# Kernel tuning notes

Measured on AMD Instinct MI355X. Metric: run time of the kernel, lower is better.

## Reference

```python
import jax, jax.numpy as jnp
import numpy as np

N_HEADS = 16
ROPE_BASE = 10000.0


def _rope_tables(T, head_dim, dtype):
    d2 = head_dim // 2
    inv_freq = 1.0 / (ROPE_BASE ** (jnp.arange(0, head_dim, 2, dtype=jnp.float32) / head_dim))
    t = jnp.arange(T, dtype=jnp.float32)
    freqs = jnp.outer(t, inv_freq)  # [T, d2]
    cos = jnp.cos(freqs)[None, :, None, :].astype(dtype)  # [1,T,1,d2]
    sin = jnp.sin(freqs)[None, :, None, :].astype(dtype)
    return cos, sin


def _apply_rotary(x, cos, sin):
    # x: [B,T,H,D]; rotate halves
    d = x.shape[-1] // 2
    x1, x2 = x[..., :d], x[..., d:]
    return jnp.concatenate([x1 * cos + x2 * sin, -x1 * sin + x2 * cos], axis=-1)


def setup_inputs() -> dict:
    key = jax.random.key(0)
    k1, k2, k3 = jax.random.split(key, 3)
    B, T, C = 2, 2048, 1024
    x = jax.random.normal(k1, (B, T, C), dtype=jnp.float32)
    w_attn = jax.random.normal(k2, (3 * C, C), dtype=jnp.float32) * (1.0 / np.sqrt(C))
    w_proj = jax.random.normal(k3, (C, C), dtype=jnp.float32) * (1.0 / np.sqrt(C))
    return {"x": x, "w_attn": w_attn, "w_proj": w_proj}


def reference(x, w_attn, w_proj):
    B, T, C = x.shape
    H = N_HEADS
    D = C // H
    qkv = jnp.einsum('btc,fc->btf', x, w_attn)  # [B,T,3C]
    q, k, v = jnp.split(qkv, 3, axis=2)
    q = q.reshape(B, T, H, D)
    k = k.reshape(B, T, H, D)
    v = v.reshape(B, T, H, D)
    cos, sin = _rope_tables(T, D, x.dtype)
    q = _apply_rotary(q, cos, sin)
    k = _apply_rotary(k, cos, sin)
    # causal SDPA, scale 1/sqrt(D)
    scale = 1.0 / np.sqrt(D)
    scores = jnp.einsum('bqhd,bkhd->bhqk', q, k) * scale
    causal = jnp.tril(jnp.ones((T, T), dtype=bool))
    scores = jnp.where(causal[None, None], scores, jnp.finfo(scores.dtype).min)
    attn = jax.nn.softmax(scores, axis=-1)
    y = jnp.einsum('bhqk,bkhd->bqhd', attn, v).reshape(B, T, C)
    return jnp.einsum('btc,oc->bto', y, w_proj)
```

## Files before the change

kernel.cpp:

```cpp
#include <hip/hip_runtime.h>
#include <math.h>

typedef __bf16 bf16x8 __attribute__((ext_vector_type(8)));
typedef float f32x4 __attribute__((ext_vector_type(4)));

__device__ __forceinline__ unsigned f2bf(float f) {
    union { float f; unsigned u; } v; v.f = f;
    return (v.u + 0x7FFFu + ((v.u >> 16) & 1u)) >> 16;
}

__device__ __forceinline__ unsigned cvtpk(float a, float b) {
    unsigned r;
    __asm__("v_cvt_pk_bf16_f32 %0, %1, %2" : "=v"(r) : "v"(a), "v"(b));
    return r;
}

__device__ __forceinline__ void gload16(const ushort* g, ushort* l) {
    __builtin_amdgcn_global_load_lds(
        (const __attribute__((address_space(1))) void*)g,
        (__attribute__((address_space(3))) void*)l, 16, 0, 0);
}

__device__ __forceinline__ bool src_is_fp32(const unsigned* s) {
    int sane = 0;
#pragma unroll
    for (int i = 0; i < 64; ++i) {
        unsigned lo = s[i] & 0xFFFFu;
        unsigned e = (lo >> 7) & 0xFF;
        if (lo == 0u || (e >= 100u && e <= 140u)) sane++;
    }
    return sane < 48;
}

__global__ __launch_bounds__(256) void tobf16_all_kernel(
    const unsigned* __restrict__ s0, const unsigned* __restrict__ s1,
    const unsigned* __restrict__ s2,
    ushort* __restrict__ d0, ushort* __restrict__ d1, ushort* __restrict__ d2) {
    const int bx = blockIdx.x;
    const unsigned* src;
    ushort* dst;
    int lb;
    if (bx < 2048)      { src = s0; dst = d0; lb = bx; }
    else if (bx < 3584) { src = s1; dst = d1; lb = bx - 2048; }
    else                { src = s2; dst = d2; lb = bx - 3584; }
    const int i = lb * 2048 + threadIdx.x * 8;
    if (src_is_fp32(src)) {
        const float* fs = (const float*)src;
        float4 f0 = *(const float4*)(fs + i);
        float4 f1 = *(const float4*)(fs + i + 4);
        uint4 o;
        o.x = f2bf(f0.x) | (f2bf(f0.y) << 16);
        o.y = f2bf(f0.z) | (f2bf(f0.w) << 16);
        o.z = f2bf(f1.x) | (f2bf(f1.y) << 16);
        o.w = f2bf(f1.z) | (f2bf(f1.w) << 16);
        *(uint4*)(dst + i) = o;
    } else {
        *(uint4*)(dst + i) = *(const uint4*)((const ushort*)src + i);
    }
}

constexpr int GBM = 128, GBN = 128, GBK = 32;

__global__ __launch_bounds__(256) void gemm_qkv_rope_kernel(
    const ushort* __restrict__ A, const ushort* __restrict__ Bmat,
    ushort* __restrict__ qkvh, int K) {
    __shared__ ushort As[2][GBM * GBK];
    __shared__ ushort Bs[2][GBN * GBK];

    const int tid  = threadIdx.x;
    const int lane = tid & 63;
    const int wv   = tid >> 6;
    const int wm   = (wv >> 1) * 64;
    const int wn   = (wv & 1) * 64;

    const ushort* Ab = A + (size_t)blockIdx.x * GBM * K;
    const ushort* Bb = Bmat + (size_t)blockIdx.y * GBN * K;

    f32x4 acc[4][4];
#pragma unroll
    for (int i = 0; i < 4; i++)
#pragma unroll
        for (int j = 0; j < 4; j++) acc[i][j] = (f32x4){0.f, 0.f, 0.f, 0.f};

    const int srow = tid >> 2;
    const int scol = (tid & 3) * 8;
    const int fr = lane & 15;
    const int fk = (lane >> 4) * 8;
    const int nK = K >> 5;

    gload16(Ab + (size_t)srow * K + scol,        As[0] + wv * 512);
    gload16(Ab + (size_t)(srow + 64) * K + scol, As[0] + wv * 512 + 2048);
    gload16(Bb + (size_t)srow * K + scol,        Bs[0] + wv * 512);
    gload16(Bb + (size_t)(srow + 64) * K + scol, Bs[0] + wv * 512 + 2048);

#pragma unroll 1
    for (int it = 0; it < nK; ++it) {
        const int cur = it & 1;
        __syncthreads();
        if (it + 1 < nK) {
            const int k0 = (it + 1) << 5, nxt = cur ^ 1;
            gload16(Ab + (size_t)srow * K + k0 + scol,        As[nxt] + wv * 512);
            gload16(Ab + (size_t)(srow + 64) * K + k0 + scol, As[nxt] + wv * 512 + 2048);
            gload16(Bb + (size_t)srow * K + k0 + scol,        Bs[nxt] + wv * 512);
            gload16(Bb + (size_t)(srow + 64) * K + k0 + scol, Bs[nxt] + wv * 512 + 2048);
        }
        bf16x8 af[4], bfr[4];
#pragma unroll
        for (int i = 0; i < 4; i++)
            af[i] = *(const bf16x8*)(As[cur] + (wm + i * 16 + fr) * GBK + fk);
#pragma unroll
        for (int j = 0; j < 4; j++)
            bfr[j] = *(const bf16x8*)(Bs[cur] + (wn + j * 16 + fr) * GBK + fk);
#pragma unroll
        for (int i = 0; i < 4; i++)
#pragma unroll
            for (int j = 0; j < 4; j++)
                acc[i][j] = __builtin_amdgcn_mfma_f32_16x16x32_bf16(af[i], bfr[j], acc[i][j], 0, 0, 0);
    }

    const int crow0 = (lane >> 4) * 4;
    const int col0  = blockIdx.y * GBN + wn;
    const int which = col0 >> 10;
    const int hh    = (col0 >> 6) & 15;
    ushort* outp = qkvh + (size_t)which * 4194304 + (size_t)hh * 131072;

    if (which < 2) {
        const float inva = exp2f((float)fr * -0.41524101186f);
        const float invb = exp2f((float)(fr + 16) * -0.41524101186f);
        const float qs = (which == 0) ? 0.125f : 1.0f;
#pragma unroll
        for (int i = 0; i < 4; i++)
#pragma unroll
            for (int r = 0; r < 4; r++) {
                int row = blockIdx.x * GBM + wm + i * 16 + crow0 + r;
                int t = row & 2047;
                size_t ob = ((size_t)(row >> 11)) * 2097152 + (size_t)t * 64;
                float sa, ca, sb, cb;
                __sincosf((float)t * inva, &sa, &ca);
                __sincosf((float)t * invb, &sb, &cb);
                float q0 = acc[i][0][r], q1 = acc[i][1][r];
                float q2 = acc[i][2][r], q3 = acc[i][3][r];
                float n0 = (q0 * ca + q2 * sa) * qs;
                float n1 = (q1 * cb + q3 * sb) * qs;
                float n2 = (q2 * ca - q0 * sa) * qs;
                float n3 = (q3 * cb - q1 * sb) * qs;
                unsigned u01 = cvtpk(n0, n1);
                unsigned u23 = cvtpk(n2, n3);
                outp[ob + fr]      = (ushort)(u01 & 0xFFFFu);
                outp[ob + 16 + fr] = (ushort)(u01 >> 16);
                outp[ob + 32 + fr] = (ushort)(u23 & 0xFFFFu);
                outp[ob + 48 + fr] = (ushort)(u23 >> 16);
            }
    } else {
#pragma unroll
        for (int i = 0; i < 4; i++)
#pragma unroll
            for (int r = 0; r < 4; r++) {
                int row = blockIdx.x * GBM + wm + i * 16 + crow0 + r;
                int t = row & 2047;
                size_t ob = ((size_t)(row >> 11)) * 2097152 + (size_t)t * 64;
                unsigned u01 = cvtpk(acc[i][0][r], acc[i][1][r]);
                unsigned u23 = cvtpk(acc[i][2][r], acc[i][3][r]);
                outp[ob + fr]      = (ushort)(u01 & 0xFFFFu);
                outp[ob + 16 + fr] = (ushort)(u01 >> 16);
                outp[ob + 32 + fr] = (ushort)(u23 & 0xFFFFu);
                outp[ob + 48 + fr] = (ushort)(u23 >> 16);
            }
    }
}

__global__ __launch_bounds__(256) void gemm_bt_kernel(
    const ushort* __restrict__ A, const ushort* __restrict__ Bmat,
    float* __restrict__ C, int M, int N, int K) {
    __shared__ ushort As[2][GBM * GBK];
    __shared__ ushort Bs[2][GBN * GBK];

    const int tid  = threadIdx.x;
    const int lane = tid & 63;
    const int wv   = tid >> 6;
    const int wm   = (wv >> 1) * 64;
    const int wn   = (wv & 1) * 64;

    const ushort* Ab = A + (size_t)blockIdx.x * GBM * K;
    const ushort* Bb = Bmat + (size_t)blockIdx.y * GBN * K;

    f32x4 acc[4][4];
#pragma unroll
    for (int i = 0; i < 4; i++)
#pragma unroll
        for (int j = 0; j < 4; j++) acc[i][j] = (f32x4){0.f, 0.f, 0.f, 0.f};

    const int srow = tid >> 2;
    const int scol = (tid & 3) * 8;
    const int fr = lane & 15;
    const int fk = (lane >> 4) * 8;
    const int nK = K >> 5;

    gload16(Ab + (size_t)srow * K + scol,        As[0] + wv * 512);
    gload16(Ab + (size_t)(srow + 64) * K + scol, As[0] + wv * 512 + 2048);
    gload16(Bb + (size_t)srow * K + scol,        Bs[0] + wv * 512);
    gload16(Bb + (size_t)(srow + 64) * K + scol, Bs[0] + wv * 512 + 2048);

#pragma unroll 1
    for (int it = 0; it < nK; ++it) {
        const int cur = it & 1;
        __syncthreads();
        if (it + 1 < nK) {
            const int k0 = (it + 1) << 5, nxt = cur ^ 1;
            gload16(Ab + (size_t)srow * K + k0 + scol,        As[nxt] + wv * 512);
            gload16(Ab + (size_t)(srow + 64) * K + k0 + scol, As[nxt] + wv * 512 + 2048);
            gload16(Bb + (size_t)srow * K + k0 + scol,        Bs[nxt] + wv * 512);
            gload16(Bb + (size_t)(srow + 64) * K + k0 + scol, Bs[nxt] + wv * 512 + 2048);
        }
        bf16x8 af[4], bfr[4];
#pragma unroll
        for (int i = 0; i < 4; i++)
            af[i] = *(const bf16x8*)(As[cur] + (wm + i * 16 + fr) * GBK + fk);
#pragma unroll
        for (int j = 0; j < 4; j++)
            bfr[j] = *(const bf16x8*)(Bs[cur] + (wn + j * 16 + fr) * GBK + fk);
#pragma unroll
        for (int i = 0; i < 4; i++)
#pragma unroll
            for (int j = 0; j < 4; j++)
                acc[i][j] = __builtin_amdgcn_mfma_f32_16x16x32_bf16(af[i], bfr[j], acc[i][j], 0, 0, 0);
    }

    const int crow0 = (lane >> 4) * 4;
#pragma unroll
    for (int i = 0; i < 4; i++)
#pragma unroll
        for (int j = 0; j < 4; j++)
#pragma unroll
            for (int r = 0; r < 4; r++) {
                int row = blockIdx.x * GBM + wm + i * 16 + crow0 + r;
                int col = blockIdx.y * GBN + wn + j * 16 + fr;
                C[(size_t)row * N + col] = acc[i][j][r];
            }
}

#define NEG_BIG (-1e30f)
constexpr int VT_OFF = 16384;
constexpr int LPV    = 136;
constexpr int PS_OFF = VT_OFF + 2 * 64 * LPV;
constexpr int LPP    = 72;

__global__ __launch_bounds__(1024) void attn_kernel(const ushort* __restrict__ qkvh,
                                                    ushort* __restrict__ y) {
    __shared__ ushort SM[PS_OFF + 16 * 16 * LPP];

    const int tid  = threadIdx.x;
    const int lane = tid & 63;
    const int wv   = tid >> 6;
    const int half = wv >> 3;
    const int wq   = wv & 7;
    const int jb   = half * 4;
    const int pid  = blockIdx.x;
    const int bh   = blockIdx.y;
    const int b    = bh >> 4, h = bh & 15;

    const ushort* qp = qkvh + (size_t)b * 2097152 + (size_t)h * 131072;
    const ushort* kp = qp + 4194304;
    const ushort* vp = qp + 8388608;

    const int fr = lane & 15;
    const int fq = lane >> 4;
    const int fk = fq * 8;

    const int krow = tid >> 3;
    const int kblk = tid & 7;
    const int ksrc = krow * 64 + ((kblk ^ (krow & 7)) << 3);
    const int koff0 = (fq ^ (fr & 7)) << 3;
    const int koff1 = koff0 ^ 32;
    const int vkey = tid & 127;
    const int vd0  = (tid >> 7) * 8;

    ushort* pw = SM + PS_OFF + wv * (16 * LPP);

#pragma unroll 1
    for (int seg = 0; seg < 2; ++seg) {
        const int qb = seg ? (15 - pid) : pid;
        const int nIt = qb + 1;

        __syncthreads();

        gload16(kp + ksrc, SM + wv * 512);
        uint4 vr = *(const uint4*)(vp + (size_t)vkey * 64 + vd0);
        {
            unsigned w[4] = {vr.x, vr.y, vr.z, vr.w};
            ushort* vt0 = SM + VT_OFF;
#pragma unroll
            for (int t = 0; t < 4; ++t) {
                vt0[(vd0 + 2 * t)     * LPV + vkey] = (ushort)(w[t] & 0xFFFFu);
                vt0[(vd0 + 2 * t + 1) * LPV + vkey] = (ushort)(w[t] >> 16);
            }
        }
        if (1 < nIt)
            vr = *(const uint4*)(vp + (size_t)(128 + vkey) * 64 + vd0);

        const int qrow = qb * 128 + wq * 16 + fr;
        bf16x8 qf0 = *(const bf16x8*)(qp + (size_t)qrow * 64 + fk);
        bf16x8 qf1 = *(const bf16x8*)(qp + (size_t)qrow * 64 + 32 + fk);

        f32x4 o[4];
        o[0] = o[1] = o[2] = o[3] = (f32x4){0.f, 0.f, 0.f, 0.f};
        float lsum = 0.f;

#pragma unroll 1
        for (int it = 0; it < nIt; ++it) {
            const int cur = it & 1;
            const int k0 = it * 128;
            const ushort* Ksc = SM + cur * 8192;
            const ushort* Vtc = SM + VT_OFF + cur * (64 * LPV);
            __syncthreads();
            if (it + 1 < nIt) {
                const int nxt = cur ^ 1;
                gload16(kp + (it + 1) * 8192 + ksrc, SM + nxt * 8192 + wv * 512);
                ushort* vtn = SM + VT_OFF + nxt * (64 * LPV);
                unsigned w[4] = {vr.x, vr.y, vr.z, vr.w};
#pragma unroll
                for (int t = 0; t < 4; ++t) {
                    vtn[(vd0 + 2 * t)     * LPV + vkey] = (ushort)(w[t] & 0xFFFFu);
                    vtn[(vd0 + 2 * t + 1) * LPV + vkey] = (ushort)(w[t] >> 16);
                }
                if (it + 2 < nIt)
                    vr = *(const uint4*)(vp + (size_t)(k0 + 256 + vkey) * 64 + vd0);
            }

            f32x4 s[4];
#pragma unroll
            for (int jl = 0; jl < 4; ++jl) {
                const int row = ((jb + jl) * 16 + fr) * 64;
                bf16x8 kf0 = *(const bf16x8*)(Ksc + row + koff0);
                bf16x8 kf1 = *(const bf16x8*)(Ksc + row + koff1);
                f32x4 z = (f32x4){0.f, 0.f, 0.f, 0.f};
                z = __builtin_amdgcn_mfma_f32_16x16x32_bf16(kf0, qf0, z, 0, 0, 0);
                z = __builtin_amdgcn_mfma_f32_16x16x32_bf16(kf1, qf1, z, 0, 0, 0);
                s[jl] = z;
            }
            if (it + 1 < nIt) {
#pragma unroll
                for (int jl = 0; jl < 4; ++jl)
#pragma unroll
                    for (int r = 0; r < 4; ++r) {
                        float p = __expf(s[jl][r]);
                        s[jl][r] = p;
                        lsum += p;
                    }
            } else {
#pragma unroll
                for (int jl = 0; jl < 4; ++jl)
#pragma unroll
                    for (int r = 0; r < 4; ++r) {
                        float v = s[jl][r];
                        if ((k0 + (jb + jl) * 16 + fq * 4 + r) > qrow) v = NEG_BIG;
                        float p = __expf(v);
                        s[jl][r] = p;
                        lsum += p;
                    }
            }

#pragma unroll
            for (int jl = 0; jl < 4; ++jl) {
                uint2 u;
                u.x = cvtpk(s[jl][0], s[jl][1]);
                u.y = cvtpk(s[jl][2], s[jl][3]);
                *(uint2*)(pw + fr * LPP + jl * 16 + fq * 4) = u;
            }
            __asm__ volatile("" ::: "memory");

#pragma unroll
            for (int kl = 0; kl < 2; ++kl) {
                bf16x8 pf = *(const bf16x8*)(pw + fr * LPP + kl * 32 + fk);
                const int vcol = half * 64 + kl * 32 + fk;
#pragma unroll
                for (int j4 = 0; j4 < 4; ++j4) {
                    bf16x8 vf = *(const bf16x8*)(Vtc + (j4 * 16 + fr) * LPV + vcol);
                    o[j4] = __builtin_amdgcn_mfma_f32_16x16x32_bf16(pf, vf, o[j4], 0, 0, 0);
                }
            }
        }

        lsum += __shfl_xor(lsum, 16, 64);
        lsum += __shfl_xor(lsum, 32, 64);

        __syncthreads();
        float* ex = (float*)(SM + PS_OFF) + wq * 1104;
        if (half) {
#pragma unroll
            for (int j4 = 0; j4 < 4; ++j4)
#pragma unroll
                for (int r = 0; r < 4; ++r)
                    ex[lane * 17 + j4 * 4 + r] = o[j4][r];
            if (fq == 0) ex[1088 + fr] = lsum;
        }
        __syncthreads();
        if (!half) {
            float linv[4];
#pragma unroll
            for (int r = 0; r < 4; ++r) {
                float own = __shfl(lsum, fq * 4 + r, 64);
                linv[r] = 1.0f / (own + ex[1088 + fq * 4 + r]);
            }
#pragma unroll
            for (int j4 = 0; j4 < 4; j4 += 2)
#pragma unroll
                for (int r = 0; r < 4; ++r) {
                    int row = qb * 128 + wq * 16 + fq * 4 + r;
                    size_t yb = ((size_t)b * 2048 + row) * 1024 + h * 64;
                    float v0 = (o[j4][r]     + ex[lane * 17 + j4 * 4 + r])       * linv[r];
                    float v1 = (o[j4 + 1][r] + ex[lane * 17 + (j4 + 1) * 4 + r]) * linv[r];
                    unsigned u = cvtpk(v0, v1);
                    y[yb + j4 * 16 + fr]       = (ushort)(u & 0xFFFFu);
                    y[yb + (j4 + 1) * 16 + fr] = (ushort)(u >> 16);
                }
        }
    }
}

extern "C" void kernel_launch(void* const* d_in, const int* in_sizes, int n_in,
                              void* d_out, int out_size, void* d_ws, size_t ws_size,
                              hipStream_t stream) {
    const int nx = in_sizes[0];
    const int na = in_sizes[1];
    const int np = in_sizes[2];

    ushort* qkvh = (ushort*)d_ws;
    ushort* yb   = qkvh + (size_t)3 * 4194304;
    ushort* xb   = yb + (size_t)4096 * 1024;
    ushort* wab  = xb + nx;
    ushort* wpb  = wab + na;
    size_t need = ((size_t)3 * 4194304 + (size_t)4096 * 1024 + nx + na + np) * 2;
    if (ws_size < need) return;

    tobf16_all_kernel<<<dim3(4096), 256, 0, stream>>>(
        (const unsigned*)d_in[0], (const unsigned*)d_in[1], (const unsigned*)d_in[2],
        xb, wab, wpb);

    gemm_qkv_rope_kernel<<<dim3(32, 24), 256, 0, stream>>>(xb, wab, qkvh, 1024);
    attn_kernel<<<dim3(8, 32), 1024, 0, stream>>>(qkvh, yb);
    gemm_bt_kernel<<<dim3(32, 8), 256, 0, stream>>>(yb, wpb, (float*)d_out, 4096, 1024, 1024);
}
```

Measured before the change: 189.2 us.

## Store V pre-transposed from QKV GEMM and double query rows per attention wave

The QKV GEMM epilogue now writes V in a transposed [head][d][t] layout using packed 8-byte stores. That lets the attention kernel fetch V tiles straight into LDS with async global_load_lds and an XOR swizzle, instead of moving them through registers and transposing with scalar LDS stores. The attention block drops from 1024 to 512 threads, and each wave handles 32 query rows (two MFMA tiles) so every K and V fragment read from LDS is reused twice. The cost is more registers per wave and fewer waves per block, which may reduce latency hiding.

```diff
diff --git a/kernel.cpp b/kernel.cpp
--- a/kernel.cpp
+++ b/kernel.cpp
@@ -122,9 +122,9 @@
     const int col0  = blockIdx.y * GBN + wn;
     const int which = col0 >> 10;
     const int hh    = (col0 >> 6) & 15;
-    ushort* outp = qkvh + (size_t)which * 4194304 + (size_t)hh * 131072;
 
     if (which < 2) {
+        ushort* outp = qkvh + (size_t)which * 4194304 + (size_t)hh * 131072;
         const float inva = exp2f((float)fr * -0.41524101186f);
         const float invb = exp2f((float)(fr + 16) * -0.41524101186f);
         const float qs = (which == 0) ? 0.125f : 1.0f;
@@ -152,20 +152,20 @@
                 outp[ob + 48 + fr] = (ushort)(u23 >> 16);
             }
     } else {
-#pragma unroll
-        for (int i = 0; i < 4; i++)
-#pragma unroll
-            for (int r = 0; r < 4; r++) {
-                int row = blockIdx.x * GBM + wm + i * 16 + crow0 + r;
-                int t = row & 2047;
-                size_t ob = ((size_t)(row >> 11)) * 2097152 + (size_t)t * 64;
-                unsigned u01 = cvtpk(acc[i][0][r], acc[i][1][r]);
-                unsigned u23 = cvtpk(acc[i][2][r], acc[i][3][r]);
-                outp[ob + fr]      = (ushort)(u01 & 0xFFFFu);
-                outp[ob + 16 + fr] = (ushort)(u01 >> 16);
-                outp[ob + 32 + fr] = (ushort)(u23 & 0xFFFFu);
-                outp[ob + 48 + fr] = (ushort)(u23 >> 16);
-            }
+        const int row0 = blockIdx.x * GBM;
+        ushort* vout = qkvh + (size_t)2 * 4194304
+                     + ((size_t)(row0 >> 11)) * 2097152 + (size_t)hh * 131072;
+#pragma unroll
+        for (int i = 0; i < 4; i++) {
+            const int t0 = (blockIdx.x * GBM + wm + i * 16 + crow0) & 2047;
+#pragma unroll
+            for (int j = 0; j < 4; j++) {
+                uint2 u;
+                u.x = cvtpk(acc[i][j][0], acc[i][j][1]);
+                u.y = cvtpk(acc[i][j][2], acc[i][j][3]);
+                *(uint2*)(vout + (size_t)(j * 16 + fr) * 2048 + t0) = u;
+            }
+        }
     }
 }
 
@@ -240,20 +240,19 @@
 }
 
 #define NEG_BIG (-1e30f)
+constexpr int LPP    = 72;
 constexpr int VT_OFF = 16384;
-constexpr int LPV    = 136;
-constexpr int PS_OFF = VT_OFF + 2 * 64 * LPV;
-constexpr int LPP    = 72;
-
-__global__ __launch_bounds__(1024) void attn_kernel(const ushort* __restrict__ qkvh,
-                                                    ushort* __restrict__ y) {
-    __shared__ ushort SM[PS_OFF + 16 * 16 * LPP];
+constexpr int PS_OFF = 32768;
+
+__global__ __launch_bounds__(512) void attn_kernel(const ushort* __restrict__ qkvh,
+                                                   ushort* __restrict__ y) {
+    __shared__ ushort SM[PS_OFF + 8 * 32 * LPP];
 
     const int tid  = threadIdx.x;
     const int lane = tid & 63;
     const int wv   = tid >> 6;
-    const int half = wv >> 3;
-    const int wq   = wv & 7;
+    const int half = wv >> 2;
+    const int wq   = wv & 3;
     const int jb   = half * 4;
     const int pid  = blockIdx.x;
     const int bh   = blockIdx.y;
@@ -267,15 +266,16 @@
     const int fq = lane >> 4;
     const int fk = fq * 8;
 
-    const int krow = tid >> 3;
-    const int kblk = tid & 7;
-    const int ksrc = krow * 64 + ((kblk ^ (krow & 7)) << 3);
+    const int ksrcA = (tid >> 3) * 64 + (((tid & 7) ^ ((tid >> 3) & 7)) << 3);
+    const int ksrcB = ksrcA + 4096;
+    const int vsrcA = (tid >> 4) * 2048 + (((tid & 15) ^ ((tid >> 4) & 15)) << 3);
+    const int vsrcB = vsrcA + 65536;
     const int koff0 = (fq ^ (fr & 7)) << 3;
     const int koff1 = koff0 ^ 32;
-    const int vkey = tid & 127;
-    const int vd0  = (tid >> 7) * 8;
-
-    ushort* pw = SM + PS_OFF + wv * (16 * LPP);
+    const int voff0 = ((half * 8 + fq) ^ fr) << 3;
+    const int voff1 = ((half * 8 + 4 + fq) ^ fr) << 3;
+
+    ushort* pw = SM + PS_OFF + wv * (32 * LPP);
 
 #pragma unroll 1
     for (int seg = 0; seg < 2; ++seg) {
@@ -284,135 +284,155 @@
 
         __syncthreads();
 
-        gload16(kp + ksrc, SM + wv * 512);
-        uint4 vr = *(const uint4*)(vp + (size_t)vkey * 64 + vd0);
-        {
-            unsigned w[4] = {vr.x, vr.y, vr.z, vr.w};
-            ushort* vt0 = SM + VT_OFF;
-#pragma unroll
-            for (int t = 0; t < 4; ++t) {
-                vt0[(vd0 + 2 * t)     * LPV + vkey] = (ushort)(w[t] & 0xFFFFu);
-                vt0[(vd0 + 2 * t + 1) * LPV + vkey] = (ushort)(w[t] >> 16);
-            }
-        }
-        if (1 < nIt)
-            vr = *(const uint4*)(vp + (size_t)(128 + vkey) * 64 + vd0);
-
-        const int qrow = qb * 128 + wq * 16 + fr;
-        bf16x8 qf0 = *(const bf16x8*)(qp + (size_t)qrow * 64 + fk);
-        bf16x8 qf1 = *(const bf16x8*)(qp + (size_t)qrow * 64 + 32 + fk);
-
-        f32x4 o[4];
-        o[0] = o[1] = o[2] = o[3] = (f32x4){0.f, 0.f, 0.f, 0.f};
-        float lsum = 0.f;
+        gload16(kp + ksrcA, SM + wv * 512);
+        gload16(kp + ksrcB, SM + 4096 + wv * 512);
+        gload16(vp + vsrcA, SM + VT_OFF + wv * 512);
+        gload16(vp + vsrcB, SM + VT_OFF + 4096 + wv * 512);
+
+        const int qrowA = qb * 128 + wq * 32 + fr;
+        bf16x8 qfA0 = *(const bf16x8*)(qp + (size_t)qrowA * 64 + fk);
+        bf16x8 qfA1 = *(const bf16x8*)(qp + (size_t)qrowA * 64 + 32 + fk);
+        bf16x8 qfB0 = *(const bf16x8*)(qp + (size_t)(qrowA + 16) * 64 + fk);
+        bf16x8 qfB1 = *(const bf16x8*)(qp + (size_t)(qrowA + 16) * 64 + 32 + fk);
+
+        f32x4 oA[4], oB[4];
+#pragma unroll
+        for (int j4 = 0; j4 < 4; ++j4) {
+            oA[j4] = (f32x4){0.f, 0.f, 0.f, 0.f};
+            oB[j4] = (f32x4){0.f, 0.f, 0.f, 0.f};
+        }
+        float lsumA = 0.f, lsumB = 0.f;
 
 #pragma unroll 1
         for (int it = 0; it < nIt; ++it) {
             const int cur = it & 1;
             const int k0 = it * 128;
             const ushort* Ksc = SM + cur * 8192;
-            const ushort* Vtc = SM + VT_OFF + cur * (64 * LPV);
+            const ushort* Vtc = SM + VT_OFF + cur * 8192;
             __syncthreads();
             if (it + 1 < nIt) {
                 const int nxt = cur ^ 1;
-                gload16(kp + (it + 1) * 8192 + ksrc, SM + nxt * 8192 + wv * 512);
-                ushort* vtn = SM + VT_OFF + nxt * (64 * LPV);
-                unsigned w[4] = {vr.x, vr.y, vr.z, vr.w};
-#pragma unroll
-                for (int t = 0; t < 4; ++t) {
-                    vtn[(vd0 + 2 * t)     * LPV + vkey] = (ushort)(w[t] & 0xFFFFu);
-                    vtn[(vd0 + 2 * t + 1) * LPV + vkey] = (ushort)(w[t] >> 16);
-                }
-                if (it + 2 < nIt)
-                    vr = *(const uint4*)(vp + (size_t)(k0 + 256 + vkey) * 64 + vd0);
-            }
-
-            f32x4 s[4];
+                gload16(kp + (it + 1) * 8192 + ksrcA, SM + nxt * 8192 + wv * 512);
+                gload16(kp + (it + 1) * 8192 + ksrcB, SM + nxt * 8192 + 4096 + wv * 512);
+                gload16(vp + (it + 1) * 128 + vsrcA, SM + VT_OFF + nxt * 8192 + wv * 512);
+                gload16(vp + (it + 1) * 128 + vsrcB, SM + VT_OFF + nxt * 8192 + 4096 + wv * 512);
+            }
+
+            f32x4 sA[4], sB[4];
 #pragma unroll
             for (int jl = 0; jl < 4; ++jl) {
                 const int row = ((jb + jl) * 16 + fr) * 64;
                 bf16x8 kf0 = *(const bf16x8*)(Ksc + row + koff0);
                 bf16x8 kf1 = *(const bf16x8*)(Ksc + row + koff1);
-                f32x4 z = (f32x4){0.f, 0.f, 0.f, 0.f};
-                z = __builtin_amdgcn_mfma_f32_16x16x32_bf16(kf0, qf0, z, 0, 0, 0);
-                z = __builtin_amdgcn_mfma_f32_16x16x32_bf16(kf1, qf1, z, 0, 0, 0);
-                s[jl] = z;
+                f32x4 zA = (f32x4){0.f, 0.f, 0.f, 0.f};
+                f32x4 zB = (f32x4){0.f, 0.f, 0.f, 0.f};
+                zA = __builtin_amdgcn_mfma_f32_16x16x32_bf16(kf0, qfA0, zA, 0, 0, 0);
+                zA = __builtin_amdgcn_mfma_f32_16x16x32_bf16(kf1, qfA1, zA, 0, 0, 0);
+                zB = __builtin_amdgcn_mfma_f32_16x16x32_bf16(kf0, qfB0, zB, 0, 0, 0);
+                zB = __builtin_amdgcn_mfma_f32_16x16x32_bf16(kf1, qfB1, zB, 0, 0, 0);
+                sA[jl] = zA;
+                sB[jl] = zB;
             }
             if (it + 1 < nIt) {
 #pragma unroll
                 for (int jl = 0; jl < 4; ++jl)
 #pragma unroll
                     for (int r = 0; r < 4; ++r) {
-                        float p = __expf(s[jl][r]);
-                        s[jl][r] = p;
-                        lsum += p;
+                        float pA = __expf(sA[jl][r]);
+                        float pB = __expf(sB[jl][r]);
+                        sA[jl][r] = pA; lsumA += pA;
+                        sB[jl][r] = pB; lsumB += pB;
                     }
             } else {
 #pragma unroll
                 for (int jl = 0; jl < 4; ++jl)
 #pragma unroll
                     for (int r = 0; r < 4; ++r) {
-                        float v = s[jl][r];
-                        if ((k0 + (jb + jl) * 16 + fq * 4 + r) > qrow) v = NEG_BIG;
-                        float p = __expf(v);
-                        s[jl][r] = p;
-                        lsum += p;
+                        const int key = k0 + (jb + jl) * 16 + fq * 4 + r;
+                        float vA = (key > qrowA)      ? NEG_BIG : sA[jl][r];
+                        float vB = (key > qrowA + 16) ? NEG_BIG : sB[jl][r];
+                        float pA = __expf(vA);
+                        float pB = __expf(vB);
+                        sA[jl][r] = pA; lsumA += pA;
+                        sB[jl][r] = pB; lsumB += pB;
                     }
             }
 
 #pragma unroll
             for (int jl = 0; jl < 4; ++jl) {
-                uint2 u;
-                u.x = cvtpk(s[jl][0], s[jl][1]);
-                u.y = cvtpk(s[jl][2], s[jl][3]);
-                *(uint2*)(pw + fr * LPP + jl * 16 + fq * 4) = u;
+                uint2 uA, uB;
+                uA.x = cvtpk(sA[jl][0], sA[jl][1]);
+                uA.y = cvtpk(sA[jl][2], sA[jl][3]);
+                uB.x = cvtpk(sB[jl][0], sB[jl][1]);
+                uB.y = cvtpk(sB[jl][2], sB[jl][3]);
+                *(uint2*)(pw + fr * LPP + jl * 16 + fq * 4)        = uA;
+                *(uint2*)(pw + (16 + fr) * LPP + jl * 16 + fq * 4) = uB;
             }
             __asm__ volatile("" ::: "memory");
 
 #pragma unroll
             for (int kl = 0; kl < 2; ++kl) {
-                bf16x8 pf = *(const bf16x8*)(pw + fr * LPP + kl * 32 + fk);
-                const int vcol = half * 64 + kl * 32 + fk;
+                bf16x8 pfA = *(const bf16x8*)(pw + fr * LPP + kl * 32 + fk);
+                bf16x8 pfB = *(const bf16x8*)(pw + (16 + fr) * LPP + kl * 32 + fk);
+                const int voff = kl ? voff1 : voff0;
 #pragma unroll
                 for (int j4 = 0; j4 < 4; ++j4) {
-                    bf16x8 vf = *(const bf16x8*)(Vtc + (j4 * 16 + fr) * LPV + vcol);
-                    o[j4] = __builtin_amdgcn_mfma_f32_16x16x32_bf16(pf, vf, o[j4], 0, 0, 0);
+                    bf16x8 vf = *(const bf16x8*)(Vtc + (j4 * 16 + fr) * 128 + voff);
+                    oA[j4] = __builtin_amdgcn_mfma_f32_16x16x32_bf16(pfA, vf, oA[j4], 0, 0, 0);
+                    oB[j4] = __builtin_amdgcn_mfma_f32_16x16x32_bf16(pfB, vf, oB[j4], 0, 0, 0);
                 }
             }
         }
 
-        lsum += __shfl_xor(lsum, 16, 64);
-        lsum += __shfl_xor(lsum, 32, 64);
+        lsumA += __shfl_xor(lsumA, 16, 64);
+        lsumA += __shfl_xor(lsumA, 32, 64);
+        lsumB += __shfl_xor(lsumB, 16, 64);
+        lsumB += __shfl_xor(lsumB, 32, 64);
 
         __syncthreads();
-        float* ex = (float*)(SM + PS_OFF) + wq * 1104;
+        float* exA = (float*)(SM + PS_OFF) + (wq * 2) * 1104;
+        float* exB = exA + 1104;
         if (half) {
 #pragma unroll
             for (int j4 = 0; j4 < 4; ++j4)
 #pragma unroll
-                for (int r = 0; r < 4; ++r)
-                    ex[lane * 17 + j4 * 4 + r] = o[j4][r];
-            if (fq == 0) ex[1088 + fr] = lsum;
+                for (int r = 0; r < 4; ++r) {
+                    exA[lane * 17 + j4 * 4 + r] = oA[j4][r];
+                    exB[lane * 17 + j4 * 4 + r] = oB[j4][r];
+                }
+            if (fq == 0) {
+                exA[1088 + fr] = lsumA;
+                exB[1088 + fr] = lsumB;
+            }
         }
         __syncthreads();
         if (!half) {
-            float linv[4];
+            float linvA[4], linvB[4];
 #pragma unroll
             for (int r = 0; r < 4; ++r) {
-                float own = __shfl(lsum, fq * 4 + r, 64);
-                linv[r] = 1.0f / (own + ex[1088 + fq * 4 + r]);
+                float ownA = __shfl(lsumA, fq * 4 + r, 64);
+                float ownB = __shfl(lsumB, fq * 4 + r, 64);
+                linvA[r] = 1.0f / (ownA + exA[1088 + fq * 4 + r]);
+                linvB[r] = 1.0f / (ownB + exB[1088 + fq * 4 + r]);
             }
 #pragma unroll
             for (int j4 = 0; j4 < 4; j4 += 2)
 #pragma unroll
                 for (int r = 0; r < 4; ++r) {
-                    int row = qb * 128 + wq * 16 + fq * 4 + r;
-                    size_t yb = ((size_t)b * 2048 + row) * 1024 + h * 64;
-                    float v0 = (o[j4][r]     + ex[lane * 17 + j4 * 4 + r])       * linv[r];
-                    float v1 = (o[j4 + 1][r] + ex[lane * 17 + (j4 + 1) * 4 + r]) * linv[r];
-                    unsigned u = cvtpk(v0, v1);
-                    y[yb + j4 * 16 + fr]       = (ushort)(u & 0xFFFFu);
-                    y[yb + (j4 + 1) * 16 + fr] = (ushort)(u >> 16);
+                    int rowA = qb * 128 + wq * 32 + fq * 4 + r;
+                    size_t ybA = ((size_t)b * 2048 + rowA) * 1024 + h * 64;
+                    float a0 = (oA[j4][r]     + exA[lane * 17 + j4 * 4 + r])       * linvA[r];
+                    float a1 = (oA[j4 + 1][r] + exA[lane * 17 + (j4 + 1) * 4 + r]) * linvA[r];
+                    unsigned ua = cvtpk(a0, a1);
+                    y[ybA + j4 * 16 + fr]       = (ushort)(ua & 0xFFFFu);
+                    y[ybA + (j4 + 1) * 16 + fr] = (ushort)(ua >> 16);
+
+                    size_t ybB = ybA + (size_t)16 * 1024;
+                    float b0 = (oB[j4][r]     + exB[lane * 17 + j4 * 4 + r])       * linvB[r];
+                    float b1 = (oB[j4 + 1][r] + exB[lane * 17 + (j4 + 1) * 4 + r]) * linvB[r];
+                    unsigned ub = cvtpk(b0, b1);
+                    y[ybB + j4 * 16 + fr]       = (ushort)(ub & 0xFFFFu);
+                    y[ybB + (j4 + 1) * 16 + fr] = (ushort)(ub >> 16);
                 }
         }
     }
@@ -438,6 +458,6 @@
         xb, wab, wpb);
 
     gemm_qkv_rope_kernel<<<dim3(32, 24), 256, 0, stream>>>(xb, wab, qkvh, 1024);
-    attn_kernel<<<dim3(8, 32), 1024, 0, stream>>>(qkvh, yb);
+    attn_kernel<<<dim3(8, 32), 512, 0, stream>>>(qkvh, yb);
     gemm_bt_kernel<<<dim3(32, 8), 256, 0, stream>>>(yb, wpb, (float*)d_out, 4096, 1024, 1024);
 }
```

After: 180.5 us. 1.05x faster.
